# Kernel tuning notes

Hardware: AMD Instinct MI355X
Metric: run time of the kernel (lower is better)

The kernel has to match this reference:

```python
import jax, jax.numpy as jnp
import numpy as np

D = 12          # tree depth; N = 2**D - 1 = 4095 nodes per tree (heap layout)
B = 64          # batch of trees
V = 128         # VOCAB_SIZE (one-hot token width)
H = 256         # hidden_size
NUM_OPS = 20
TEMP = 3.0      # self.temperature


def setup_inputs() -> dict:
    key = jax.random.key(0)
    ks = jax.random.split(key, 9)
    s = 0.02
    return {
        "arg_hot": jax.random.uniform(ks[0], (B, 2**D - 1, V), dtype=jnp.float32),
        "Wiou": jax.random.normal(ks[1], (V, 3 * H), dtype=jnp.float32) * s,
        "biou": jnp.zeros((3 * H,), jnp.float32),
        "Uiou": jax.random.normal(ks[2], (2, H, 3 * H), dtype=jnp.float32) * s,
        "Wf": jax.random.normal(ks[3], (V, H), dtype=jnp.float32) * s,
        "bf": jnp.zeros((H,), jnp.float32),
        "Uf": jax.random.normal(ks[4], (2, 2, H, H), dtype=jnp.float32) * s,
        "actor_w": jax.random.normal(ks[5], (NUM_OPS, H), dtype=jnp.float32) * s,
        "actor_b": jnp.zeros((NUM_OPS,), jnp.float32),
        "validity_mask": jnp.ones((B, NUM_OPS), jnp.float32),
    }


def _binary_tree_lstm(arg_hot, Wiou, biou, Uiou, Wf, bf, Uf):
    """Levelized apply_binary_lstm: bottom-up N-ary (N=2) Tree-LSTM over a
    complete binary tree stored in heap order (children of node j at level l
    are positions 2j, 2j+1 of level l+1). Missing children (below leaves)
    contribute zero hidden/cell states, matching self.tz in the original."""
    Bn = arg_hot.shape[0]
    h_child = c_child = None
    h = c = None
    for l in reversed(range(D)):
        m = 2 ** l
        x = arg_hot[:, m - 1: 2 * m - 1]                    # [B, m, V]
        if h_child is None:  # leaf level: zero child states
            hk = jnp.zeros((2, Bn, m, H), arg_hot.dtype)
            ck = hk
        else:                # children 2j, 2j+1 are adjacent pairs
            hk = h_child.reshape(Bn, m, 2, H).transpose(2, 0, 1, 3)  # [2,B,m,H]
            ck = c_child.reshape(Bn, m, 2, H).transpose(2, 0, 1, 3)
        iou = (jnp.einsum('bmv,vg->bmg', x, Wiou) + biou
               + jnp.einsum('kbmh,khg->bmg', hk, Uiou))     # [B,m,3H]
        i, o, u = jnp.split(iou, 3, axis=-1)
        i, o, u = jax.nn.sigmoid(i), jax.nn.sigmoid(o), jnp.tanh(u)
        # per-child forget gates f_k = sigma(Wf x + sum_j Uf[k,j] h_j + bf)
        f = jax.nn.sigmoid(jnp.einsum('bmv,vh->bmh', x, Wf) + bf
                           + jnp.einsum('jbmh,kjhd->kbmd', hk, Uf))  # [2,B,m,H]
        c = i * u + jnp.sum(f * ck, axis=0)                 # [B,m,H]
        h = o * jnp.tanh(c)
        h_child, c_child = h, c
    return h[:, 0], c[:, 0]                                  # root states [B,H]


def reference(arg_hot, Wiou, biou, Uiou, Wf, bf, Uf, actor_w, actor_b, validity_mask):
    root_h, _ = _binary_tree_lstm(arg_hot, Wiou, biou, Uiou, Wf, bf, Uf)
    # external-actor branch of policy(): mask weights/bias, add log-mask, tempered softmax
    w = actor_w[None, :, :] * validity_mask[:, :, None]      # [B,O,H]
    b = actor_b[None, :] * validity_mask                     # [B,O]
    logits = jnp.log(validity_mask) + jnp.einsum('bh,boh->bo', root_h, w) + b
    return jax.nn.softmax(logits / TEMP, axis=-1)
```

## Files before the change

### kernel.cpp

```cpp
#include <hip/hip_runtime.h>
#include <hip/hip_bf16.h>
#include <math.h>

typedef __hip_bfloat16 bf16;
typedef float f32x4 __attribute__((ext_vector_type(4)));
typedef short bf16x8 __attribute__((ext_vector_type(8)));

#define NNODES 4095
#define BATCH 64
#define NUM_OPS 20
#define TEMP 3.0f

#define OFF_WTILE 0x000000ull
#define OFF_BIAS  0x190000ull
#define OFF_HA    0x200000ull
#define OFF_CA    (OFF_HA + (64ull<<20))
#define OFF_HB    (OFF_CA + (64ull<<20))
#define OFF_CB    (OFF_HB + (32ull<<20))

__device__ __forceinline__ float sigmoid_f(float x) {
    return 1.0f / (1.0f + __expf(-x));
}
__device__ __forceinline__ float tanh_f(float x) {
    return 1.0f - 2.0f / (__expf(2.0f * x) + 1.0f);
}

__device__ __forceinline__ void async_copy16(const bf16* g, bf16* l) {
    __builtin_amdgcn_global_load_lds(
        (const __attribute__((address_space(1))) void*)g,
        (__attribute__((address_space(3))) void*)l,
        16, 0, 0);
}

__global__ void init_weights(const float* __restrict__ Wiou,
                             const float* __restrict__ biou,
                             const float* __restrict__ Uiou,
                             const float* __restrict__ Wf,
                             const float* __restrict__ bfv,
                             const float* __restrict__ Uf,
                             bf16* __restrict__ wtile,
                             float* __restrict__ biasCat)
{
    int idx = blockIdx.x * 256 + threadIdx.x;
    if (idx < 1280 * 640) {
        int k = idx % 640;
        int n = idx / 640;
        int g = n >> 8;
        int ch = n & 255;
        float v;
        if (k < 128) {
            v = (g < 3) ? Wiou[k * 768 + n] : Wf[k * 256 + ch];
        } else {
            int par = (k < 384) ? 0 : 1;
            int hh = (k - 128) & 255;
            if (g < 3) v = Uiou[(par * 256 + hh) * 768 + n];
            else {
                int kk = g - 3;
                v = Uf[(((kk * 2 + par) * 256) + hh) * 256 + ch];
            }
        }
        int chblk = (ch >> 5);
        int cl    = ch & 31;
        int kb    = k >> 6;
        int chunk = (k & 63) >> 3;
        int e     = k & 7;
        int brow  = g * 32 + cl;
        size_t dst = ((size_t)(chblk * 10 + kb) * 8 + chunk) * 1280 + brow * 8 + e;
        wtile[dst] = __float2bfloat16(v);
    }
    if (idx < 1280) {
        biasCat[idx] = (idx < 768) ? biou[idx] : bfv[idx & 255];
    }
}

template <bool LEAF>
__global__ __launch_bounds__(256, 4)
void level_kernel(const float* __restrict__ arg_hot,
                  const bf16* __restrict__ wtile,
                  const float* __restrict__ biasCat,
                  const bf16* __restrict__ h_child,
                  const bf16* __restrict__ c_child,
                  bf16* __restrict__ h_out,
                  bf16* __restrict__ c_out,
                  int m, int logm)
{
    constexpr int NG = LEAF ? 3 : 5;
    constexpr int KI = LEAF ? 2 : 10;

    const int M = BATCH * m;
    const int node_base = m - 1;

    __shared__ bf16 As[128 * 64];
    __shared__ bf16 Bs[8 * 160 * 8];

    const int tid = threadIdx.x;

    int bid = blockIdx.x;
    int mtiles = gridDim.x >> 3;
    int mtile, chblk;
    if ((mtiles & 7) == 0) {
        int xcd = bid & 7;
        int seq = bid >> 3;
        chblk = seq & 7;
        mtile = ((seq >> 3) << 3) + xcd;
    } else {
        mtile = bid >> 3;
        chblk = bid & 7;
    }
    const int rbase  = mtile * 128;
    const int chbase = chblk * 32;

    const int lane = tid & 63;
    const int wave = tid >> 6;
    const int wr = wave & 1;
    const int wc = wave >> 1;
    const int l15 = lane & 15;
    const int lq  = lane >> 4;
    const int xr7 = l15 & 7;

    f32x4 acc[4][NG];
#pragma unroll
    for (int a = 0; a < 4; ++a)
#pragma unroll
        for (int g = 0; g < NG; ++g)
            acc[a][g] = (f32x4){0.f, 0.f, 0.f, 0.f};

    const int row_l = lane >> 3;
    const int cc_l  = lane & 7;
    const int aoff  = row_l * 512 + (cc_l ^ row_l) * 8;

    const bf16* wbase = wtile + (size_t)(chblk * 10) * 10240;

    const int arow = tid & 127;
    const int rs = min(rbase + arow, M - 1);
    const float* xrow = arg_hot +
        ((size_t)(rs >> logm) * NNODES + node_base + (rs & (m - 1))) * 128;
    const int xswz_base = arow * 64;
    const int ar7 = arow & 7;

    for (int kb = 0; kb < KI; ++kb) {
        if (LEAF || kb < 2) {
            const float* xk = xrow + kb * 64;
#pragma unroll
            for (int j = 0; j < 4; ++j) {
                int chunk = (tid >> 7) + 2 * j;
                const float* src = xk + chunk * 8;
                float4 a = *(const float4*)src;
                float4 b = *(const float4*)(src + 4);
                union { int4 i4; __hip_bfloat162 h2[4]; } u;
                u.h2[0] = __float22bfloat162_rn(make_float2(a.x, a.y));
                u.h2[1] = __float22bfloat162_rn(make_float2(a.z, a.w));
                u.h2[2] = __float22bfloat162_rn(make_float2(b.x, b.y));
                u.h2[3] = __float22bfloat162_rn(make_float2(b.z, b.w));
                *(int4*)&As[xswz_base + ((chunk ^ ar7) * 8)] = u.i4;
            }
        } else {
            const bf16* hb = h_child + (size_t)rbase * 512 + (kb * 64 - 128) + aoff;
#pragma unroll
            for (int i = 0; i < 4; ++i) {
                int t = wave * 4 + i;
                async_copy16(hb + t * 8 * 512, &As[t * 512]);
            }
        }
        {
            const bf16* bsrc = wbase + (size_t)kb * 10240;
#pragma unroll
            for (int i = 0; i < 5; ++i) {
                int t = wave * 5 + i;
                async_copy16(bsrc + t * 512 + lane * 8, &Bs[t * 512]);
            }
        }
        __syncthreads();
#pragma unroll
        for (int ks = 0; ks < 2; ++ks) {
            int q = ks * 4 + lq;
            int qa = (q ^ xr7) * 8;
            bf16x8 af[4];
#pragma unroll
            for (int rt = 0; rt < 4; ++rt)
                af[rt] = *(const bf16x8*)&As[(wr * 64 + rt * 16 + l15) * 64 + qa];
#pragma unroll
            for (int g = 0; g < NG; ++g) {
                bf16x8 bfr = *(const bf16x8*)&Bs[q * 1280 + (g * 32 + wc * 16 + l15) * 8];
#pragma unroll
                for (int rt = 0; rt < 4; ++rt)
                    acc[rt][g] = __builtin_amdgcn_mfma_f32_16x16x32_bf16(
                        af[rt], bfr, acc[rt][g], 0, 0, 0);
            }
        }
        __syncthreads();
    }

    const int ch = chbase + wc * 16 + l15;
    const float b_i = biasCat[ch];
    const float b_o = biasCat[256 + ch];
    const float b_u = biasCat[512 + ch];
    const float b_f = LEAF ? 0.f : biasCat[768 + ch];

#pragma unroll
    for (int rt = 0; rt < 4; ++rt) {
#pragma unroll
        for (int ri = 0; ri < 4; ++ri) {
            int r = rbase + wr * 64 + rt * 16 + lq * 4 + ri;
            if (r < M) {
                float i = sigmoid_f(acc[rt][0][ri] + b_i);
                float o = sigmoid_f(acc[rt][1][ri] + b_o);
                float u = tanh_f(acc[rt][2][ri] + b_u);
                float cn;
                if (LEAF) {
                    cn = i * u;
                } else {
                    float f0 = sigmoid_f(acc[rt][3][ri] + b_f);
                    float f1 = sigmoid_f(acc[rt][4][ri] + b_f);
                    float c0 = __bfloat162float(c_child[(size_t)r * 512 + ch]);
                    float c1 = __bfloat162float(c_child[(size_t)r * 512 + 256 + ch]);
                    cn = i * u + f0 * c0 + f1 * c1;
                }
                float h = o * tanh_f(cn);
                h_out[(size_t)r * 256 + ch] = __float2bfloat16(h);
                c_out[(size_t)r * 256 + ch] = __float2bfloat16(cn);
            }
        }
    }
}

__global__ void head_kernel(const bf16* __restrict__ rootH,
                            const float* __restrict__ actor_w,
                            const float* __restrict__ actor_b,
                            const float* __restrict__ vmask,
                            float* __restrict__ out)
{
    int b = blockIdx.x;
    __shared__ float logits[NUM_OPS];
    int t = threadIdx.x;
    if (t < NUM_OPS) {
        const bf16* hr = rootH + b * 256;
        const float* w = actor_w + t * 256;
        float dot = 0.f;
        for (int hh = 0; hh < 256; ++hh)
            dot += __bfloat162float(hr[hh]) * w[hh];
        float mk = vmask[b * NUM_OPS + t];
        float lg = (mk > 0.f) ? (logf(mk) + (dot + actor_b[t]) * mk) : -INFINITY;
        logits[t] = lg / TEMP;
    }
    __syncthreads();
    if (t == 0) {
        float mx = -INFINITY;
        for (int o = 0; o < NUM_OPS; ++o) mx = fmaxf(mx, logits[o]);
        float s = 0.f;
        float e[NUM_OPS];
        for (int o = 0; o < NUM_OPS; ++o) { e[o] = __expf(logits[o] - mx); s += e[o]; }
        float inv = 1.f / s;
        for (int o = 0; o < NUM_OPS; ++o) out[b * NUM_OPS + o] = e[o] * inv;
    }
}

extern "C" void kernel_launch(void* const* d_in, const int* in_sizes, int n_in,
                              void* d_out, int out_size, void* d_ws, size_t ws_size,
                              hipStream_t stream)
{
    const float* arg_hot = (const float*)d_in[0];
    const float* Wiou    = (const float*)d_in[1];
    const float* biou    = (const float*)d_in[2];
    const float* Uiou    = (const float*)d_in[3];
    const float* Wf      = (const float*)d_in[4];
    const float* bfv     = (const float*)d_in[5];
    const float* Uf      = (const float*)d_in[6];
    const float* actor_w = (const float*)d_in[7];
    const float* actor_b = (const float*)d_in[8];
    const float* vmask   = (const float*)d_in[9];

    char* ws = (char*)d_ws;
    bf16*  wtile   = (bf16*)(ws + OFF_WTILE);
    float* biasCat = (float*)(ws + OFF_BIAS);
    bf16*  hA = (bf16*)(ws + OFF_HA);
    bf16*  cA = (bf16*)(ws + OFF_CA);
    bf16*  hB = (bf16*)(ws + OFF_HB);
    bf16*  cB = (bf16*)(ws + OFF_CB);

    init_weights<<<dim3((1280 * 640 + 255) / 256), 256, 0, stream>>>(
        Wiou, biou, Uiou, Wf, bfv, Uf, wtile, biasCat);

    {
        int m = 2048;
        int mtiles = (BATCH * m + 127) / 128;
        level_kernel<true><<<dim3(mtiles * 8), 256, 0, stream>>>(
            arg_hot, wtile, biasCat, nullptr, nullptr, hA, cA, m, 11);
    }
    for (int l = 10; l >= 0; --l) {
        int m = 1 << l;
        int mtiles = (BATCH * m + 127) / 128;
        bf16 *hc, *cc, *ho, *co;
        if (l & 1) { hc = hB; cc = cB; ho = hA; co = cA; }
        else       { hc = hA; cc = cA; ho = hB; co = cB; }
        level_kernel<false><<<dim3(mtiles * 8), 256, 0, stream>>>(
            arg_hot, wtile, biasCat, hc, cc, ho, co, m, l);
    }
    head_kernel<<<dim3(BATCH), 64, 0, stream>>>(hB, actor_w, actor_b, vmask, (float*)d_out);
}
```

Baseline: 902.4 us.

## Pre-convert leaf inputs to bf16 and use compact leaf weight tile

Adds a convert_x kernel that converts the leaf-level fp32 one-hot inputs to bf16 once, in a contiguous layout. The leaf level_kernel then loads them with async global-to-LDS copies instead of per-thread fp32 loads and conversion. It also builds a separate compact weight tile holding only the three Wiou gates, so each leaf block fetches 96 rows of B instead of 160 and uses less LDS. The trade-off is an extra launch and an extra pass over the leaf inputs. The xL buffer reuses the hB region, which the leaf level does not write.

```diff
diff --git a/kernel.cpp b/kernel.cpp
--- a/kernel.cpp
+++ b/kernel.cpp
@@ -12,11 +12,13 @@
 #define TEMP 3.0f
 
 #define OFF_WTILE 0x000000ull
-#define OFF_BIAS  0x190000ull
+#define OFF_WTL   0x190000ull
+#define OFF_BIAS  0x1C0000ull
 #define OFF_HA    0x200000ull
 #define OFF_CA    (OFF_HA + (64ull<<20))
 #define OFF_HB    (OFF_CA + (64ull<<20))
 #define OFF_CB    (OFF_HB + (32ull<<20))
+#define OFF_XL    OFF_HB
 
 __device__ __forceinline__ float sigmoid_f(float x) {
     return 1.0f / (1.0f + __expf(-x));
@@ -39,6 +41,7 @@
                              const float* __restrict__ bfv,
                              const float* __restrict__ Uf,
                              bf16* __restrict__ wtile,
+                             bf16* __restrict__ wtL,
                              float* __restrict__ biasCat)
 {
     int idx = blockIdx.x * 256 + threadIdx.x;
@@ -59,39 +62,62 @@
                 v = Uf[(((kk * 2 + par) * 256) + hh) * 256 + ch];
             }
         }
+        bf16 bv = __float2bfloat16(v);
         int chblk = (ch >> 5);
         int cl    = ch & 31;
         int kb    = k >> 6;
         int chunk = (k & 63) >> 3;
         int e     = k & 7;
         int brow  = g * 32 + cl;
-        size_t dst = ((size_t)(chblk * 10 + kb) * 8 + chunk) * 1280 + brow * 8 + e;
-        wtile[dst] = __float2bfloat16(v);
+        wtile[((size_t)(chblk * 10 + kb) * 8 + chunk) * 1280 + brow * 8 + e] = bv;
+        if (k < 128 && g < 3)
+            wtL[((size_t)(chblk * 2 + kb) * 8 + chunk) * 768 + brow * 8 + e] = bv;
     }
     if (idx < 1280) {
         biasCat[idx] = (idx < 768) ? biou[idx] : bfv[idx & 255];
     }
+}
+
+__global__ void convert_x(const float* __restrict__ arg_hot, bf16* __restrict__ xL)
+{
+    int t = blockIdx.x * 256 + threadIdx.x;
+    int row = t >> 4;
+    int ch0 = (t & 15) * 8;
+    int b = row >> 11;
+    int j = row & 2047;
+    const float* src = arg_hot + ((size_t)b * NNODES + 2047 + j) * 128 + ch0;
+    float4 a = *(const float4*)src;
+    float4 c = *(const float4*)(src + 4);
+    union { bf16x8 v; __hip_bfloat162 h2[4]; } u;
+    u.h2[0] = __float22bfloat162_rn(make_float2(a.x, a.y));
+    u.h2[1] = __float22bfloat162_rn(make_float2(a.z, a.w));
+    u.h2[2] = __float22bfloat162_rn(make_float2(c.x, c.y));
+    u.h2[3] = __float22bfloat162_rn(make_float2(c.z, c.w));
+    *(bf16x8*)(xL + (size_t)t * 8) = u.v;
 }
 
 template <bool LEAF>
 __global__ __launch_bounds__(256, 4)
 void level_kernel(const float* __restrict__ arg_hot,
-                  const bf16* __restrict__ wtile,
+                  const bf16* __restrict__ wt,
                   const float* __restrict__ biasCat,
+                  const bf16* __restrict__ xL,
                   const bf16* __restrict__ h_child,
                   const bf16* __restrict__ c_child,
                   bf16* __restrict__ h_out,
                   bf16* __restrict__ c_out,
                   int m, int logm)
 {
-    constexpr int NG = LEAF ? 3 : 5;
-    constexpr int KI = LEAF ? 2 : 10;
+    constexpr int NG  = LEAF ? 3 : 5;
+    constexpr int KI  = LEAF ? 2 : 10;
+    constexpr int BR  = LEAF ? 96 : 160;
+    constexpr int NBW = LEAF ? 3 : 5;
 
     const int M = BATCH * m;
     const int node_base = m - 1;
 
     __shared__ bf16 As[128 * 64];
-    __shared__ bf16 Bs[8 * 160 * 8];
+    __shared__ bf16 Bs[8 * BR * 8];
 
     const int tid = threadIdx.x;
 
@@ -127,19 +153,29 @@
 
     const int row_l = lane >> 3;
     const int cc_l  = lane & 7;
-    const int aoff  = row_l * 512 + (cc_l ^ row_l) * 8;
-
-    const bf16* wbase = wtile + (size_t)(chblk * 10) * 10240;
+    const int aoffH = row_l * 512 + (cc_l ^ row_l) * 8;
+    const int aoffX = row_l * 128 + (cc_l ^ row_l) * 8;
+
+    const bf16* wbase = wt + (size_t)chblk * KI * (BR * 64);
 
     const int arow = tid & 127;
     const int rs = min(rbase + arow, M - 1);
-    const float* xrow = arg_hot +
+    const float* xrow = LEAF ? nullptr : arg_hot +
         ((size_t)(rs >> logm) * NNODES + node_base + (rs & (m - 1))) * 128;
     const int xswz_base = arow * 64;
     const int ar7 = arow & 7;
 
+    const bf16* xLbase = LEAF ? xL + (size_t)rbase * 128 + aoffX : nullptr;
+
     for (int kb = 0; kb < KI; ++kb) {
-        if (LEAF || kb < 2) {
+        if (LEAF) {
+            const bf16* xb = xLbase + kb * 64;
+#pragma unroll
+            for (int i = 0; i < 4; ++i) {
+                int t = wave * 4 + i;
+                async_copy16(xb + t * 1024, &As[t * 512]);
+            }
+        } else if (kb < 2) {
             const float* xk = xrow + kb * 64;
 #pragma unroll
             for (int j = 0; j < 4; ++j) {
@@ -155,7 +191,7 @@
                 *(int4*)&As[xswz_base + ((chunk ^ ar7) * 8)] = u.i4;
             }
         } else {
-            const bf16* hb = h_child + (size_t)rbase * 512 + (kb * 64 - 128) + aoff;
+            const bf16* hb = h_child + (size_t)rbase * 512 + (kb * 64 - 128) + aoffH;
 #pragma unroll
             for (int i = 0; i < 4; ++i) {
                 int t = wave * 4 + i;
@@ -163,10 +199,10 @@
             }
         }
         {
-            const bf16* bsrc = wbase + (size_t)kb * 10240;
-#pragma unroll
-            for (int i = 0; i < 5; ++i) {
-                int t = wave * 5 + i;
+            const bf16* bsrc = wbase + (size_t)kb * (BR * 64);
+#pragma unroll
+            for (int i = 0; i < NBW; ++i) {
+                int t = wave * NBW + i;
                 async_copy16(bsrc + t * 512 + lane * 8, &Bs[t * 512]);
             }
         }
@@ -181,7 +217,7 @@
                 af[rt] = *(const bf16x8*)&As[(wr * 64 + rt * 16 + l15) * 64 + qa];
 #pragma unroll
             for (int g = 0; g < NG; ++g) {
-                bf16x8 bfr = *(const bf16x8*)&Bs[q * 1280 + (g * 32 + wc * 16 + l15) * 8];
+                bf16x8 bfr = *(const bf16x8*)&Bs[q * (BR * 8) + (g * 32 + wc * 16 + l15) * 8];
 #pragma unroll
                 for (int rt = 0; rt < 4; ++rt)
                     acc[rt][g] = __builtin_amdgcn_mfma_f32_16x16x32_bf16(
@@ -272,20 +308,23 @@
 
     char* ws = (char*)d_ws;
     bf16*  wtile   = (bf16*)(ws + OFF_WTILE);
+    bf16*  wtL     = (bf16*)(ws + OFF_WTL);
     float* biasCat = (float*)(ws + OFF_BIAS);
     bf16*  hA = (bf16*)(ws + OFF_HA);
     bf16*  cA = (bf16*)(ws + OFF_CA);
     bf16*  hB = (bf16*)(ws + OFF_HB);
     bf16*  cB = (bf16*)(ws + OFF_CB);
+    bf16*  xL = (bf16*)(ws + OFF_XL);
 
     init_weights<<<dim3((1280 * 640 + 255) / 256), 256, 0, stream>>>(
-        Wiou, biou, Uiou, Wf, bfv, Uf, wtile, biasCat);
+        Wiou, biou, Uiou, Wf, bfv, Uf, wtile, wtL, biasCat);
+    convert_x<<<dim3(8192), 256, 0, stream>>>(arg_hot, xL);
 
     {
         int m = 2048;
         int mtiles = (BATCH * m + 127) / 128;
         level_kernel<true><<<dim3(mtiles * 8), 256, 0, stream>>>(
-            arg_hot, wtile, biasCat, nullptr, nullptr, hA, cA, m, 11);
+            arg_hot, wtL, biasCat, xL, nullptr, nullptr, hA, cA, m, 11);
     }
     for (int l = 10; l >= 0; --l) {
         int m = 1 << l;
@@ -294,7 +333,7 @@
         if (l & 1) { hc = hB; cc = cB; ho = hA; co = cA; }
         else       { hc = hA; cc = cA; ho = hB; co = cB; }
         level_kernel<false><<<dim3(mtiles * 8), 256, 0, stream>>>(
-            arg_hot, wtile, biasCat, hc, cc, ho, co, m, l);
+            arg_hot, wtile, biasCat, nullptr, hc, cc, ho, co, m, l);
     }
     head_kernel<<<dim3(BATCH), 64, 0, stream>>>(hB, actor_w, actor_b, vmask, (float*)d_out);
 }
```

Result: faster. 853.1 us (-5.5%).
